# Kernel tuning notes

Measured on AMD Instinct MI355X. Metric: run time of the kernel, lower is better.

Reference implementation:

```python
import jax, jax.numpy as jnp
import numpy as np

B, T, I, H = 64, 2048, 256, 256

def setup_inputs() -> dict:
    key = jax.random.key(0)
    k1, k2, k3, k4, k5 = jax.random.split(key, 5)
    s = 1.0 / np.sqrt(H)
    return {
        "x": jax.random.normal(k1, (B, T, I), dtype=jnp.float32),
        "weight_ih": jax.random.normal(k2, (3 * H, I), dtype=jnp.float32) * s,
        "weight_hh": jax.random.normal(k3, (3 * H, H), dtype=jnp.float32) * s,
        "bias_ih": jax.random.normal(k4, (3 * H,), dtype=jnp.float32) * s,
        "bias_hh": jax.random.normal(k5, (3 * H,), dtype=jnp.float32) * s,
    }

def reference(x, weight_ih, weight_hh, bias_ih, bias_hh):
    # x: [B, T, I] (batch_first). Permute to time-major, scan GRU cell.
    xt = jnp.swapaxes(x, 0, 1)  # [T, B, I]
    # Precompute input-side gate projections for all timesteps: [T, B, 3H]
    gi_all = jnp.einsum('tbi,gi->tbg', xt, weight_ih) + bias_ih
    h0 = jnp.zeros((x.shape[0], H), dtype=x.dtype)

    def step(h, gi):
        gh = h @ weight_hh.T + bias_hh  # [B, 3H]
        i_r, i_z, i_n = jnp.split(gi, 3, axis=-1)
        h_r, h_z, h_n = jnp.split(gh, 3, axis=-1)
        r = jax.nn.sigmoid(i_r + h_r)
        z = jax.nn.sigmoid(i_z + h_z)
        n = jnp.tanh(i_n + r * h_n)
        h_new = (1.0 - z) * n + z * h
        return h_new, None

    h_final, _ = jax.lax.scan(step, h0, gi_all)
    return h_final  # return_sequences=False, return_state=False -> last hidden [B, H]
```

## Files before the change

kernel.cpp:

```cpp
#include <hip/hip_runtime.h>
#include <hip/hip_fp16.h>

typedef _Float16 h2 __attribute__((ext_vector_type(2)));
typedef _Float16 h8 __attribute__((ext_vector_type(8)));
typedef float f4 __attribute__((ext_vector_type(4)));

static constexpr int TT = 2048;
static constexpr int BB = 64;
static constexpr int II = 256;
static constexpr int HH = 256;
static constexpr int G3 = 768;

static __device__ __forceinline__ unsigned int pk2(float a, float b) {
    return __builtin_bit_cast(unsigned int, __builtin_amdgcn_cvt_pkrtz(a, b));
}

__global__ void cast_wih(const float* __restrict__ w, _Float16* __restrict__ o, int n) {
    int i = blockIdx.x * blockDim.x + threadIdx.x;
    if (i < n) o[i] = (_Float16)w[i];
}

__global__ void gi_gemm(const float* __restrict__ x, const _Float16* __restrict__ wih,
                        const float* __restrict__ bih, _Float16* __restrict__ gi) {
    const int lane = threadIdx.x & 63;
    const int wid  = threadIdx.x >> 6;
    const int gt   = blockIdx.x * 4 + wid;
    const int nt   = gt % 12;
    const int mt   = gt / 12;
    const int m0   = mt * 64;
    const int n0   = nt * 64;
    const int lr   = lane & 15;
    const int kg   = (lane >> 4) * 8;

    f4 acc[4][4] = {};

    #pragma unroll
    for (int kk = 0; kk < 256; kk += 32) {
        h8 af[4];
        h8 bf[4];
        #pragma unroll
        for (int m = 0; m < 4; ++m) {
            const float* ap = x + (size_t)(m0 + m * 16 + lr) * 256 + kk + kg;
            f4 lo = *(const f4*)ap;
            f4 hi = *(const f4*)(ap + 4);
            uint4 uu;
            uu.x = pk2(lo.x, lo.y);
            uu.y = pk2(lo.z, lo.w);
            uu.z = pk2(hi.x, hi.y);
            uu.w = pk2(hi.z, hi.w);
            af[m] = __builtin_bit_cast(h8, uu);
        }
        #pragma unroll
        for (int n = 0; n < 4; ++n) {
            bf[n] = *(const h8*)(wih + (size_t)(n0 + n * 16 + lr) * 256 + kk + kg);
        }
        #pragma unroll
        for (int m = 0; m < 4; ++m) {
            #pragma unroll
            for (int n = 0; n < 4; ++n) {
                acc[m][n] = __builtin_amdgcn_mfma_f32_16x16x32_f16(af[m], bf[n], acc[m][n], 0, 0, 0);
            }
        }
    }

    const int rg = (lane >> 4) * 4;
    #pragma unroll
    for (int n = 0; n < 4; ++n) {
        const int col = n0 + n * 16 + lr;
        const float bv = bih[col];
        #pragma unroll
        for (int m = 0; m < 4; ++m) {
            #pragma unroll
            for (int r = 0; r < 4; ++r) {
                const int row = m0 + m * 16 + rg + r;
                gi[(size_t)row * G3 + col] = (_Float16)(acc[m][n][r] + bv);
            }
        }
    }
}

__global__ __launch_bounds__(768, 3) void gru_scan(
        const _Float16* __restrict__ gi, const float* __restrict__ whh,
        const float* __restrict__ bhh, float* __restrict__ out) {
    __shared__ alignas(16) unsigned int hpk[128];
    __shared__ float ghl[768];
    __shared__ float hf[256];

    const int b   = blockIdx.x;
    const int tid = threadIdx.x;

    unsigned int wpk[128];
    {
        const f4* wrow = (const f4*)(whh + (size_t)tid * 256);
        #pragma unroll
        for (int i = 0; i < 64; ++i) {
            f4 w = wrow[i];
            wpk[2 * i]     = pk2(w.x, w.y);
            wpk[2 * i + 1] = pk2(w.z, w.w);
        }
    }
    const float bias = bhh[tid];

    if (tid < 128) hpk[tid] = 0u;
    if (tid < 256) hf[tid] = 0.f;

    const _Float16* gb = gi + (size_t)b * TT * G3;
    float gr = 0.f, gz = 0.f, gn = 0.f;
    if (tid < 256) {
        gr = (float)gb[tid];
        gz = (float)gb[256 + tid];
        gn = (float)gb[512 + tid];
    }
    __syncthreads();

    for (int t = 0; t < TT; ++t) {
        float pr = 0.f, pz = 0.f, pn = 0.f;
        if (tid < 256 && t + 1 < TT) {
            const _Float16* g2 = gb + (size_t)(t + 1) * G3;
            pr = (float)g2[tid];
            pz = (float)g2[256 + tid];
            pn = (float)g2[512 + tid];
        }

        float a0 = 0.f, a1 = 0.f, a2 = 0.f, a3 = 0.f;
        #pragma unroll
        for (int i = 0; i < 32; ++i) {
            uint4 hv = *(const uint4*)&hpk[i * 4];
            a0 = __builtin_amdgcn_fdot2(__builtin_bit_cast(h2, wpk[4 * i + 0]),
                                        __builtin_bit_cast(h2, hv.x), a0, false);
            a1 = __builtin_amdgcn_fdot2(__builtin_bit_cast(h2, wpk[4 * i + 1]),
                                        __builtin_bit_cast(h2, hv.y), a1, false);
            a2 = __builtin_amdgcn_fdot2(__builtin_bit_cast(h2, wpk[4 * i + 2]),
                                        __builtin_bit_cast(h2, hv.z), a2, false);
            a3 = __builtin_amdgcn_fdot2(__builtin_bit_cast(h2, wpk[4 * i + 3]),
                                        __builtin_bit_cast(h2, hv.w), a3, false);
        }
        ghl[tid] = ((a0 + a1) + (a2 + a3)) + bias;
        __syncthreads();

        if (tid < 256) {
            const float xr = gr + ghl[tid];
            const float xz = gz + ghl[256 + tid];
            const float r = __builtin_amdgcn_rcpf(1.f + __expf(-xr));
            const float z = __builtin_amdgcn_rcpf(1.f + __expf(-xz));
            const float xn = gn + r * ghl[512 + tid];
            const float th = 1.f - 2.f * __builtin_amdgcn_rcpf(__expf(2.f * xn) + 1.f);
            const float h0 = hf[tid];
            const float hn = (1.f - z) * th + z * h0;
            hf[tid] = hn;
            ((_Float16*)hpk)[tid] = (_Float16)hn;
            gr = pr; gz = pz; gn = pn;
        }
        __syncthreads();
    }

    if (tid < 256) out[(size_t)b * HH + tid] = hf[tid];
}

extern "C" void kernel_launch(void* const* d_in, const int* in_sizes, int n_in,
                              void* d_out, int out_size, void* d_ws, size_t ws_size,
                              hipStream_t stream) {
    const float* x   = (const float*)d_in[0];
    const float* wih = (const float*)d_in[1];
    const float* whh = (const float*)d_in[2];
    const float* bih = (const float*)d_in[3];
    const float* bhh = (const float*)d_in[4];
    float* out = (float*)d_out;

    _Float16* wih_h = (_Float16*)d_ws;
    _Float16* gi    = (_Float16*)((char*)d_ws + 512 * 1024);

    cast_wih<<<768, 256, 0, stream>>>(wih, wih_h, G3 * II);
    gi_gemm<<<6144, 256, 0, stream>>>(x, wih_h, bih, gi);
    gru_scan<<<BB, 768, 0, stream>>>(gi, whh, bhh, out);
}
```

Baseline: 2.843 ms.

## Split recurrent matvec across 8-lane groups with swizzle reduction and deeper prefetch

Changes the GRU scan's hidden-weight matvec so that each group of 8 lanes shares 8 output rows, each lane covering a 32-element K slice. Each thread therefore reads 16 words of h from LDS per step instead of all 128, which cuts LDS broadcast traffic. Partial sums are combined with ds_swizzle, and lane 0 of each group writes the results. The hidden state now stays in a register instead of shared memory, the gi prefetch runs two steps ahead, and the bias add moves into the gate math. The cost is extra swizzle reduction latency on every timestep, and dropping the launch-bounds occupancy hint may change register allocation.

```diff
diff --git a/kernel.cpp b/kernel.cpp
--- a/kernel.cpp
+++ b/kernel.cpp
@@ -4,6 +4,7 @@
 typedef _Float16 h2 __attribute__((ext_vector_type(2)));
 typedef _Float16 h8 __attribute__((ext_vector_type(8)));
 typedef float f4 __attribute__((ext_vector_type(4)));
+typedef unsigned int uv16 __attribute__((ext_vector_type(16)));
 
 static constexpr int TT = 2048;
 static constexpr int BB = 64;
@@ -13,6 +14,14 @@
 
 static __device__ __forceinline__ unsigned int pk2(float a, float b) {
     return __builtin_bit_cast(unsigned int, __builtin_amdgcn_cvt_pkrtz(a, b));
+}
+static __device__ __forceinline__ float fdot2u(unsigned int w, unsigned int h, float acc) {
+    return __builtin_amdgcn_fdot2(__builtin_bit_cast(h2, w), __builtin_bit_cast(h2, h), acc, false);
+}
+template <int OFF>
+static __device__ __forceinline__ float swz_add(float s) {
+    int v = __builtin_amdgcn_ds_swizzle(__builtin_bit_cast(int, s), OFF);
+    return s + __builtin_bit_cast(float, v);
 }
 
 __global__ void cast_wih(const float* __restrict__ w, _Float16* __restrict__ o, int n) {
@@ -79,82 +88,106 @@
     }
 }
 
-__global__ __launch_bounds__(768, 3) void gru_scan(
+__global__ __launch_bounds__(768) void gru_scan(
         const _Float16* __restrict__ gi, const float* __restrict__ whh,
         const float* __restrict__ bhh, float* __restrict__ out) {
     __shared__ alignas(16) unsigned int hpk[128];
     __shared__ float ghl[768];
-    __shared__ float hf[256];
-
-    const int b   = blockIdx.x;
-    const int tid = threadIdx.x;
-
-    unsigned int wpk[128];
-    {
-        const f4* wrow = (const f4*)(whh + (size_t)tid * 256);
-        #pragma unroll
-        for (int i = 0; i < 64; ++i) {
-            f4 w = wrow[i];
-            wpk[2 * i]     = pk2(w.x, w.y);
-            wpk[2 * i + 1] = pk2(w.z, w.w);
-        }
-    }
-    const float bias = bhh[tid];
+
+    const int b    = blockIdx.x;
+    const int tid  = threadIdx.x;
+    const int sub  = tid & 7;
+    const int rbase = (tid >> 3) * 8;
+
+    auto loadrow = [&](int j) -> uv16 {
+        const f4* wp = (const f4*)(whh + (size_t)(rbase + j) * 256 + sub * 32);
+        uv16 W;
+        #pragma unroll
+        for (int i = 0; i < 8; ++i) {
+            f4 v = wp[i];
+            W[2 * i]     = pk2(v.x, v.y);
+            W[2 * i + 1] = pk2(v.z, v.w);
+        }
+        return W;
+    };
+    const uv16 w0 = loadrow(0), w1 = loadrow(1), w2 = loadrow(2), w3 = loadrow(3),
+               w4 = loadrow(4), w5 = loadrow(5), w6 = loadrow(6), w7 = loadrow(7);
 
     if (tid < 128) hpk[tid] = 0u;
-    if (tid < 256) hf[tid] = 0.f;
 
     const _Float16* gb = gi + (size_t)b * TT * G3;
-    float gr = 0.f, gz = 0.f, gn = 0.f;
+    float b_r = 0.f, b_z = 0.f, b_n = 0.f;
+    float c_r = 0.f, c_z = 0.f, c_n = 0.f;
+    float n_r = 0.f, n_z = 0.f, n_n = 0.f;
+    float hcur = 0.f;
     if (tid < 256) {
-        gr = (float)gb[tid];
-        gz = (float)gb[256 + tid];
-        gn = (float)gb[512 + tid];
+        b_r = bhh[tid];
+        b_z = bhh[256 + tid];
+        b_n = bhh[512 + tid];
+        c_r = (float)gb[tid];
+        c_z = (float)gb[256 + tid];
+        c_n = (float)gb[512 + tid];
+        n_r = (float)gb[G3 + tid];
+        n_z = (float)gb[G3 + 256 + tid];
+        n_n = (float)gb[G3 + 512 + tid];
     }
     __syncthreads();
 
     for (int t = 0; t < TT; ++t) {
-        float pr = 0.f, pz = 0.f, pn = 0.f;
-        if (tid < 256 && t + 1 < TT) {
-            const _Float16* g2 = gb + (size_t)(t + 1) * G3;
-            pr = (float)g2[tid];
-            pz = (float)g2[256 + tid];
-            pn = (float)g2[512 + tid];
-        }
-
-        float a0 = 0.f, a1 = 0.f, a2 = 0.f, a3 = 0.f;
-        #pragma unroll
-        for (int i = 0; i < 32; ++i) {
-            uint4 hv = *(const uint4*)&hpk[i * 4];
-            a0 = __builtin_amdgcn_fdot2(__builtin_bit_cast(h2, wpk[4 * i + 0]),
-                                        __builtin_bit_cast(h2, hv.x), a0, false);
-            a1 = __builtin_amdgcn_fdot2(__builtin_bit_cast(h2, wpk[4 * i + 1]),
-                                        __builtin_bit_cast(h2, hv.y), a1, false);
-            a2 = __builtin_amdgcn_fdot2(__builtin_bit_cast(h2, wpk[4 * i + 2]),
-                                        __builtin_bit_cast(h2, hv.z), a2, false);
-            a3 = __builtin_amdgcn_fdot2(__builtin_bit_cast(h2, wpk[4 * i + 3]),
-                                        __builtin_bit_cast(h2, hv.w), a3, false);
-        }
-        ghl[tid] = ((a0 + a1) + (a2 + a3)) + bias;
+        float p_r = 0.f, p_z = 0.f, p_n = 0.f;
+        if (tid < 256 && t + 2 < TT) {
+            const _Float16* g2 = gb + (size_t)(t + 2) * G3;
+            p_r = (float)g2[tid];
+            p_z = (float)g2[256 + tid];
+            p_n = (float)g2[512 + tid];
+        }
+
+        const uint4* hp = (const uint4*)&hpk[sub * 16];
+        const uint4 hq0 = hp[0], hq1 = hp[1], hq2 = hp[2], hq3 = hp[3];
+
+        auto dotrow = [&](uv16 W) -> float {
+            float a0 = 0.f, a1 = 0.f, a2 = 0.f, a3 = 0.f;
+            a0 = fdot2u(W[0],  hq0.x, a0); a1 = fdot2u(W[1],  hq0.y, a1);
+            a2 = fdot2u(W[2],  hq0.z, a2); a3 = fdot2u(W[3],  hq0.w, a3);
+            a0 = fdot2u(W[4],  hq1.x, a0); a1 = fdot2u(W[5],  hq1.y, a1);
+            a2 = fdot2u(W[6],  hq1.z, a2); a3 = fdot2u(W[7],  hq1.w, a3);
+            a0 = fdot2u(W[8],  hq2.x, a0); a1 = fdot2u(W[9],  hq2.y, a1);
+            a2 = fdot2u(W[10], hq2.z, a2); a3 = fdot2u(W[11], hq2.w, a3);
+            a0 = fdot2u(W[12], hq3.x, a0); a1 = fdot2u(W[13], hq3.y, a1);
+            a2 = fdot2u(W[14], hq3.z, a2); a3 = fdot2u(W[15], hq3.w, a3);
+            return (a0 + a1) + (a2 + a3);
+        };
+        float s0 = dotrow(w0), s1 = dotrow(w1), s2 = dotrow(w2), s3 = dotrow(w3),
+              s4 = dotrow(w4), s5 = dotrow(w5), s6 = dotrow(w6), s7 = dotrow(w7);
+
+        #define RED(S) S = swz_add<0x041F>(S); S = swz_add<0x081F>(S); S = swz_add<0x101F>(S);
+        RED(s0) RED(s1) RED(s2) RED(s3) RED(s4) RED(s5) RED(s6) RED(s7)
+        #undef RED
+
+        if (sub == 0) {
+            ghl[rbase + 0] = s0; ghl[rbase + 1] = s1;
+            ghl[rbase + 2] = s2; ghl[rbase + 3] = s3;
+            ghl[rbase + 4] = s4; ghl[rbase + 5] = s5;
+            ghl[rbase + 6] = s6; ghl[rbase + 7] = s7;
+        }
         __syncthreads();
 
         if (tid < 256) {
-            const float xr = gr + ghl[tid];
-            const float xz = gz + ghl[256 + tid];
+            const float xr = c_r + b_r + ghl[tid];
+            const float xz = c_z + b_z + ghl[256 + tid];
             const float r = __builtin_amdgcn_rcpf(1.f + __expf(-xr));
             const float z = __builtin_amdgcn_rcpf(1.f + __expf(-xz));
-            const float xn = gn + r * ghl[512 + tid];
+            const float xn = c_n + r * (ghl[512 + tid] + b_n);
             const float th = 1.f - 2.f * __builtin_amdgcn_rcpf(__expf(2.f * xn) + 1.f);
-            const float h0 = hf[tid];
-            const float hn = (1.f - z) * th + z * h0;
-            hf[tid] = hn;
-            ((_Float16*)hpk)[tid] = (_Float16)hn;
-            gr = pr; gz = pz; gn = pn;
+            hcur = (1.f - z) * th + z * hcur;
+            ((_Float16*)hpk)[tid] = (_Float16)hcur;
+            c_r = n_r; c_z = n_z; c_n = n_n;
+            n_r = p_r; n_z = p_z; n_n = p_n;
         }
         __syncthreads();
     }
 
-    if (tid < 256) out[(size_t)b * HH + tid] = hf[tid];
+    if (tid < 256) out[(size_t)b * HH + tid] = hcur;
 }
 
 extern "C" void kernel_launch(void* const* d_in, const int* in_sizes, int n_in,
```

Measured after the change: 5.407 ms. +90.2%, slower.
